# Performance work log

Hardware: AMD Instinct MI355X
Metric: run time of the kernel (lower is better)

Reference implementation:

```python
import jax, jax.numpy as jnp
import numpy as np

N_DIS = 5000
N_GEN = 20000
N = N_DIS + N_GEN
E = 400000
N_MIRNA = 2000
EMB = 128
HID = 64


def setup_inputs() -> dict:
    key = jax.random.key(0)
    ks = jax.random.split(key, 20)
    def g(k, shape, scale=0.05):
        return jax.random.normal(k, shape, dtype=jnp.float32) * scale
    return {
        'd_features': g(ks[0], (N_DIS, 383), 1.0),
        'g_features': g(ks[1], (N_GEN, 4395), 1.0),
        'miRNA_dis': jax.random.uniform(ks[2], (N_MIRNA, N_DIS), dtype=jnp.float32),
        'gene_dis': jax.random.uniform(ks[3], (N_GEN, N_DIS), dtype=jnp.float32),
        'Wd': g(ks[4], (383, EMB)),
        'bd': jnp.zeros((EMB,), jnp.float32),
        'Wg': g(ks[5], (4395, EMB)),
        'bg': jnp.zeros((EMB,), jnp.float32),
        'W1': g(ks[6], (N_MIRNA, EMB)),
        'W4': g(ks[7], (N_DIS, EMB)),
        'Ws1': g(ks[8], (EMB, HID)),
        'Wn1': g(ks[9], (EMB, HID)),
        'b1': jnp.zeros((HID,), jnp.float32),
        'Ws2': g(ks[10], (HID, HID)),
        'Wn2': g(ks[11], (HID, HID)),
        'b2': jnp.zeros((HID,), jnp.float32),
        'src': jax.random.randint(ks[12], (E,), 0, N, dtype=jnp.int32),
        'dst': jax.random.randint(ks[13], (E,), 0, N, dtype=jnp.int32),
    }


def _sage_mean(h, src, dst, Ws, Wn, b):
    # DGL SAGEConv 'mean': fc_self(h) + fc_neigh(mean over in-neighbors) + bias
    msg = h[src]                                            # [E, d] gather
    agg = jax.ops.segment_sum(msg, dst, num_segments=N)     # [N, d] scatter-add
    deg = jax.ops.segment_sum(jnp.ones((dst.shape[0],), h.dtype), dst, num_segments=N)
    neigh = agg / jnp.maximum(deg, 1.0)[:, None]            # mean (zero-deg -> 0)
    return h @ Ws + neigh @ Wn + b


def reference(d_features, g_features, miRNA_dis, gene_dis, Wd, bd, Wg, bg,
              W1, W4, Ws1, Wn1, b1, Ws2, Wn2, b2, src, dst):
    # CrossCompressUnit outputs used by forward: A2 = M1^T W1, B1 = M2 W4
    A2 = miRNA_dis.T @ W1          # [N_DIS, EMB]
    B1 = gene_dis @ W4             # [N_GEN, EMB]
    # Node embeddings (dropout is identity at inference; torch.no_grad block)
    h_dis = 0.9 * (d_features @ Wd + bd) + 0.1 * A2   # [N_DIS, EMB]
    h_gen = 0.9 * (g_features @ Wg + bg) + 0.1 * B1   # [N_GEN, EMB]
    h = jnp.concatenate([h_dis, h_gen], axis=0)        # [N, EMB]
    h = _sage_mean(h, src, dst, Ws1, Wn1, b1)          # [N, 64]
    h = jax.nn.relu(h)
    h = _sage_mean(h, src, dst, Ws2, Wn2, b2)          # [N, 64]
    return h
```

## Files before the change

kernel.cpp:

```cpp
#include <hip/hip_runtime.h>

#define NDIS 5000
#define NGEN 20000
#define NTOT 25000
#define EDG  400000

typedef __attribute__((ext_vector_type(8))) short short8;
typedef __attribute__((ext_vector_type(4))) float f32x4;
typedef __attribute__((ext_vector_type(4), aligned(4))) float f32x4u;
typedef __attribute__((ext_vector_type(4))) unsigned int uint4v;
typedef __attribute__((ext_vector_type(2))) unsigned int uint2v;
typedef __attribute__((ext_vector_type(2), aligned(4))) unsigned int uint2a;

constexpr size_t AL(size_t x) { return (x + 255) & ~(size_t)255; }
constexpr size_t OFF_H0   = 0;
constexpr size_t OFF_PQ   = AL(OFF_H0  + (size_t)NTOT * 128 * 4);
constexpr size_t OFF_H1   = AL(OFF_PQ  + (size_t)NTOT * 128 * 4);
constexpr size_t OFF_DEG  = AL(OFF_H1  + (size_t)NTOT * 128 * 4);
constexpr size_t OFF_RS   = AL(OFF_DEG + (size_t)NTOT * 4);
constexpr size_t OFF_CUR  = AL(OFF_RS  + (size_t)(NTOT + 1) * 4);
constexpr size_t OFF_ESRC = AL(OFF_CUR + (size_t)NTOT * 4);
constexpr size_t OFF_MIT  = AL(OFF_ESRC + (size_t)EDG * 4);
constexpr size_t OFF_BDIS = AL(OFF_MIT + (size_t)5000 * 2048 * 2);
constexpr size_t OFF_BGEN = AL(OFF_BDIS + (size_t)8 * 76 * 512 * 2);
constexpr size_t OFF_BS1  = AL(OFF_BGEN + (size_t)8 * 300 * 512 * 2);
constexpr size_t OFF_BS2  = AL(OFF_BS1 + (size_t)8 * 4 * 512 * 2);

__device__ __forceinline__ ushort f2bf(float f) {
    unsigned u = __float_as_uint(f);
    u += 0x7fffu + ((u >> 16) & 1u);
    return (ushort)(u >> 16);
}

__device__ __forceinline__ unsigned cvtpk(float a, float b) {
    unsigned r;
    asm("v_cvt_pk_bf16_f32 %0, %1, %2" : "=v"(r) : "v"(a), "v"(b));
    return r;
}

__device__ __forceinline__ void MFMA(f32x4& d, short8 a, short8 b) {
    asm volatile("v_mfma_f32_16x16x32_bf16 %0, %1, %2, %0"
                 : "+v"(d) : "v"(a), "v"(b));
}

struct TcvtIns { const float* p[9]; };

__global__ __launch_bounds__(256) void k_tcvt_multi(TcvtIns ins, char* ws)
{
    constexpr int   TR[9]   = {383, 2000, 4395, 5000, 2000, 128, 128, 64, 64};
    constexpr int   TC[9]   = {128, 128, 128, 128, 5000, 64, 64, 64, 64};
    constexpr int   TKT[9]  = {76, 76, 300, 300, 2048 , 4, 4, 4, 4};
    constexpr int   TKO[9]  = {0, 12, 0, 140, 0, 0, 0, 0, 0};
    constexpr int   TRP[9]  = {384, 2048, 4480, 5120, 2048, 128, 128, 128, 128};
    constexpr int   TNOFF[9]= {0, 0, 0, 0, 0, 0, 64, 0, 64};
    constexpr int   TMODE[9]= {1, 1, 1, 1, 0, 1, 1, 1, 1};
    constexpr float TSC[9]  = {0.9f, 0.1f, 0.9f, 0.1f, 1.f, 1.f, 1.f, 1.f, 1.f};
    constexpr size_t TOUT[9]= {OFF_BDIS, OFF_BDIS, OFF_BGEN, OFF_BGEN, OFF_MIT,
                               OFF_BS1, OFF_BS1, OFF_BS2, OFF_BS2};
    constexpr int TNBX[9]   = {4, 4, 4, 4, 157, 2, 2, 2, 2};
    constexpr int PRE[10]   = {0, 48, 304, 864, 1504, 11552, 11560, 11568, 11576, 11584};

    int bid = blockIdx.x;
    int d = 0;
#pragma unroll
    for (int q = 1; q < 9; ++q) if (bid >= PRE[q]) d = q;
    int local = bid - PRE[d];
    int bx = local % TNBX[d], by = local / TNBX[d];
    const int R = TR[d], C = TC[d], KT = TKT[d], KO = TKO[d];
    const int Rp = TRP[d], noff = TNOFF[d];
    const float scale = TSC[d];
    const float* in = ins.p[d];
    ushort* out = (ushort*)(ws + TOUT[d]);

    __shared__ float t[32][33];
    int tx = threadIdx.x & 31, ty = threadIdx.x >> 5;
    int c0 = bx * 32, r0 = by * 32;
#pragma unroll
    for (int j = 0; j < 4; ++j) {
        int r = r0 + ty + j * 8, c = c0 + tx;
        t[ty + j * 8][tx] = (r < R && c < C) ? in[(size_t)r * C + c] : 0.f;
    }
    __syncthreads();
#pragma unroll
    for (int j = 0; j < 4; ++j) {
        int c = c0 + ty + j * 8, r = r0 + tx;
        if (c >= C || r >= Rp) continue;
        ushort bv = f2bf(scale * t[tx][ty + j * 8]);
        if (TMODE[d] == 0) {
            out[(size_t)c * KT + r] = bv;
        } else {
            int n = noff + c, k = r;
            out[(size_t)((n >> 4) * KT + KO + (k >> 5)) * 512 +
                ((k >> 3) & 3) * 128 + (n & 15) * 8 + (k & 7)] = bv;
        }
    }
}

template<int A2MODE, bool ATOMIC>
__global__ __launch_bounds__(256, 2) void gemm_st(
    const float* __restrict__ A1, int lda1, int K1, int nst1,
    const void* __restrict__ A2v, int lda2, int K2, int nst2,
    const ushort* __restrict__ Bf, int KT,
    float* __restrict__ C, int M, const float* __restrict__ bias)
{
    __shared__ ushort lds0[64 * 128];
    __shared__ ushort lds1[64 * 128];
    const int tid  = threadIdx.x;
    const int lane = tid & 63;
    const int w    = tid >> 6;
    const int fr = lane & 15, kq = lane >> 4;
    const int bm0 = blockIdx.x * 64;

    const int NSTT = nst1 + nst2;
    const int per = (NSTT + gridDim.y - 1) / gridDim.y;
    const int s0 = blockIdx.y * per;
    const int s1 = min(NSTT, s0 + per);
    const int NT = s1 - s0;
    if (NT <= 0) return;

    f32x4 acc[4][2];
#pragma unroll
    for (int i = 0; i < 4; ++i) { acc[i][0] = {0.f,0.f,0.f,0.f}; acc[i][1] = {0.f,0.f,0.f,0.f}; }

    uint4v faA[8], faB[8];
    short8 Breg0[4][2], Breg1[4][2];

    const int srow = w * 16 + (lane >> 5);
    const int scol = lane & 31;

    auto issueA = [&](int stg, uint4v* fa) {
        const bool r1 = (A2MODE == 0) || (stg < nst1);
#pragma unroll
        for (int i = 0; i < 8; ++i) {
            int r = bm0 + srow + i * 2;
            if (r > M - 1) r = M - 1;
            if (r1) {
                const int kb = stg << 7;
                const int k = kb + scol * 4;
                const float* p = A1 + (size_t)r * lda1 + k;
                if (kb + 128 <= K1) {
                    fa[i] = __builtin_bit_cast(uint4v, *(const f32x4u*)p);
                } else {
                    f32x4 v;
#pragma unroll
                    for (int e = 0; e < 4; ++e) v[e] = (k + e < K1) ? p[e] : 0.f;
                    fa[i] = __builtin_bit_cast(uint4v, v);
                }
            } else if (A2MODE == 1) {
                const int kb = (stg - nst1) << 7;
                const int kc = kb + scol * 4;
                const float* p = (const float*)A2v + (size_t)r * lda2 + kc;
                if (kb + 128 <= K2) {
                    fa[i] = __builtin_bit_cast(uint4v, *(const f32x4u*)p);
                } else {
                    f32x4 v;
#pragma unroll
                    for (int e = 0; e < 4; ++e) v[e] = (kc + e < K2) ? p[e] : 0.f;
                    fa[i] = __builtin_bit_cast(uint4v, v);
                }
            } else {
                const int kc = ((stg - nst1) << 7) + scol * 4;
                uint2a v = *(const uint2a*)((const ushort*)A2v + (size_t)r * lda2 + kc);
                fa[i][0] = v[0]; fa[i][1] = v[1];
            }
        }
    };
    auto issueB = [&](int stg, short8 (*BR)[2]) {
#pragma unroll
        for (int ks = 0; ks < 4; ++ks)
#pragma unroll
            for (int nf = 0; nf < 2; ++nf)
                BR[ks][nf] = *(const short8*)(
                    Bf + (size_t)((w * 2 + nf) * KT + stg * 4 + ks) * 512 + lane * 8);
    };
    auto writeT = [&](int stg, const uint4v* fa, ushort* buf) {
        const bool cvt = (A2MODE != 2) || (stg < nst1);
        const int G = scol >> 1, h = lane & 1;
#pragma unroll
        for (int i = 0; i < 8; ++i) {
            int r = srow + i * 2;
            const size_t off = (size_t)r * 256 + ((G ^ (r & 7)) << 4) + h * 8;
            uint2v d;
            if (cvt) {
                f32x4 v = __builtin_bit_cast(f32x4, fa[i]);
                d[0] = cvtpk(v[0], v[1]);
                d[1] = cvtpk(v[2], v[3]);
            } else {
                d[0] = fa[i][0]; d[1] = fa[i][1];
            }
            *(uint2v*)((char*)buf + off) = d;
        }
    };

#define PHASE(T, BR, LDSC, FAW, LDSW)                                        \
    {                                                                        \
        const int x7 = fr & 7;                                               \
        _Pragma("unroll")                                                    \
        for (int ks = 0; ks < 4; ++ks) {                                     \
            short8 af[4];                                                    \
            _Pragma("unroll")                                                \
            for (int mf = 0; mf < 4; ++mf)                                   \
                af[mf] = *(const short8*)&LDSC[fr * 128 + mf * 2048 +        \
                                              (((ks * 4 + kq) ^ x7) << 3)];  \
            _Pragma("unroll")                                                \
            for (int mf = 0; mf < 4; ++mf) {                                 \
                MFMA(acc[mf][0], af[mf], BR[ks][0]);                         \
                MFMA(acc[mf][1], af[mf], BR[ks][1]);                         \
            }                                                                \
        }                                                                    \
        if ((T) + 2 < NT) issueB(s0 + (T) + 2, BR);                          \
        __builtin_amdgcn_s_barrier();                                        \
        if ((T) + 1 < NT) {                                                  \
            writeT(s0 + (T) + 1, FAW, LDSW);                                 \
            if ((T) + 3 < NT) issueA(s0 + (T) + 3, FAW);                     \
            asm volatile("s_waitcnt lgkmcnt(0)" ::: "memory");               \
            __builtin_amdgcn_s_barrier();                                    \
        }                                                                    \
    }

    issueA(s0, faA); issueB(s0, Breg0);
    if (NT > 1) { issueA(s0 + 1, faB); issueB(s0 + 1, Breg1); }
    writeT(s0, faA, lds0);
    if (NT > 2) issueA(s0 + 2, faA);
    asm volatile("s_waitcnt lgkmcnt(0)" ::: "memory");
    __builtin_amdgcn_s_barrier();

    for (int t = 0; t < NT; t += 2) {
        PHASE(t, Breg0, lds0, faB, lds1);
        if (t + 1 < NT) PHASE(t + 1, Breg1, lds1, faA, lds0);
    }
#undef PHASE

    asm volatile("s_nop 7\n\ts_nop 7\n\ts_nop 7" ::: "memory");
#pragma unroll
    for (int mf = 0; mf < 4; ++mf)
#pragma unroll
        for (int nf = 0; nf < 2; ++nf)
#pragma unroll
            for (int r = 0; r < 4; ++r) {
                int row = bm0 + mf * 16 + kq * 4 + r;
                if (row < M) {
                    int col = w * 32 + nf * 16 + fr;
                    if (ATOMIC) {
                        atomicAdd(&C[(size_t)row * 128 + col], acc[mf][nf][r]);
                    } else {
                        float v = acc[mf][nf][r];
                        if (col < 64) v += bias[col];
                        C[(size_t)row * 128 + col] = v;
                    }
                }
            }
}

__global__ void k_binit(float* __restrict__ h0, const float* __restrict__ bd,
                        const float* __restrict__ bg) {
    int i = blockIdx.x * 256 + threadIdx.x;
    if (i >= NTOT * 128) return;
    int col = i & 127;
    h0[i] = 0.9f * ((i >> 7) < NDIS ? bd[col] : bg[col]);
}

__global__ void k_deg(const int* __restrict__ dst, int* __restrict__ deg, int E) {
    int e = blockIdx.x * blockDim.x + threadIdx.x;
    if (e < E) atomicAdd(&deg[dst[e]], 1);
}

__global__ __launch_bounds__(1024) void k_scan(const int* __restrict__ deg,
                                               int* __restrict__ row_start,
                                               int* __restrict__ cursor, int n) {
    __shared__ int wsum[16];
    __shared__ int carry_s;
    int t = threadIdx.x;
    int lane = t & 63, wid = t >> 6;
    if (t == 0) { carry_s = 0; row_start[0] = 0; }
    __syncthreads();
    for (int base = 0; base < n; base += 1024) {
        int i = base + t;
        int v = (i < n) ? deg[i] : 0;
        int x = v;
#pragma unroll
        for (int off = 1; off < 64; off <<= 1) {
            int y = __shfl_up(x, off, 64);
            if (lane >= off) x += y;
        }
        if (lane == 63) wsum[wid] = x;
        __syncthreads();
        if (wid == 0) {
            int s = (lane < 16) ? wsum[lane] : 0;
#pragma unroll
            for (int off = 1; off < 16; off <<= 1) {
                int y = __shfl_up(s, off, 64);
                if (lane >= off) s += y;
            }
            if (lane < 16) wsum[lane] = s;
        }
        __syncthreads();
        int pre = (wid > 0 ? wsum[wid - 1] : 0) + carry_s;
        int incl = x + pre;
        if (i < n) { row_start[i + 1] = incl; cursor[i] = incl - v; }
        __syncthreads();
        if (t == 1023) carry_s = incl;
        __syncthreads();
    }
}

__global__ void k_fill(const int* __restrict__ src, const int* __restrict__ dst,
                       int* __restrict__ cursor, int* __restrict__ esrc, int E) {
    int e = blockIdx.x * blockDim.x + threadIdx.x;
    if (e < E) {
        int pos = atomicAdd(&cursor[dst[e]], 1);
        esrc[pos] = src[e];
    }
}

__global__ __launch_bounds__(64) void k_agg(const float* __restrict__ PQ,
                                            const int* __restrict__ rs,
                                            const int* __restrict__ esrc,
                                            float* __restrict__ out, int ldout, int relu)
{
    int n = blockIdx.x, t = threadIdx.x;
    int s0 = rs[n], s1 = rs[n + 1];
    float a0 = 0.f, a1 = 0.f, a2 = 0.f, a3 = 0.f;
    int i = s0;
    for (; i + 4 <= s1; i += 4) {
        int e0 = esrc[i], e1 = esrc[i + 1], e2 = esrc[i + 2], e3 = esrc[i + 3];
        a0 += PQ[(size_t)e0 * 128 + 64 + t];
        a1 += PQ[(size_t)e1 * 128 + 64 + t];
        a2 += PQ[(size_t)e2 * 128 + 64 + t];
        a3 += PQ[(size_t)e3 * 128 + 64 + t];
    }
    for (; i < s1; ++i) a0 += PQ[(size_t)esrc[i] * 128 + 64 + t];
    float s = (a0 + a1) + (a2 + a3);
    float dg = (float)(s1 - s0);
    s /= fmaxf(dg, 1.f);
    float v = PQ[(size_t)n * 128 + t] + s;
    if (relu) v = fmaxf(v, 0.f);
    out[(size_t)n * ldout + t] = v;
}

extern "C" void kernel_launch(void* const* d_in, const int* in_sizes, int n_in,
                              void* d_out, int out_size, void* d_ws, size_t ws_size,
                              hipStream_t stream)
{
    const float* d_features = (const float*)d_in[0];
    const float* g_features = (const float*)d_in[1];
    const float* miRNA_dis  = (const float*)d_in[2];
    const float* gene_dis   = (const float*)d_in[3];
    const float* Wd  = (const float*)d_in[4];
    const float* bd  = (const float*)d_in[5];
    const float* Wg  = (const float*)d_in[6];
    const float* bg  = (const float*)d_in[7];
    const float* W1  = (const float*)d_in[8];
    const float* W4  = (const float*)d_in[9];
    const float* Ws1 = (const float*)d_in[10];
    const float* Wn1 = (const float*)d_in[11];
    const float* b1  = (const float*)d_in[12];
    const float* Ws2 = (const float*)d_in[13];
    const float* Wn2 = (const float*)d_in[14];
    const float* b2  = (const float*)d_in[15];
    const int* src = (const int*)d_in[16];
    const int* dst = (const int*)d_in[17];
    (void)in_sizes; (void)n_in; (void)out_size; (void)ws_size;

    char* ws = (char*)d_ws;
    float*  h0   = (float*)(ws + OFF_H0);
    float*  PQ   = (float*)(ws + OFF_PQ);
    float*  h1   = (float*)(ws + OFF_H1);
    int*    deg  = (int*)(ws + OFF_DEG);
    int*    rs   = (int*)(ws + OFF_RS);
    int*    cur  = (int*)(ws + OFF_CUR);
    int*    esrc = (int*)(ws + OFF_ESRC);
    ushort* miT  = (ushort*)(ws + OFF_MIT);
    ushort* Bdis = (ushort*)(ws + OFF_BDIS);
    ushort* Bgen = (ushort*)(ws + OFF_BGEN);
    ushort* Bs1  = (ushort*)(ws + OFF_BS1);
    ushort* Bs2  = (ushort*)(ws + OFF_BS2);

    hipMemsetAsync(deg, 0, (size_t)NTOT * 4, stream);
    hipMemsetAsync(h1, 0, (size_t)NTOT * 128 * 4, stream);
    k_deg<<<(EDG + 255) / 256, 256, 0, stream>>>(dst, deg, EDG);
    k_scan<<<1, 1024, 0, stream>>>(deg, rs, cur, NTOT);
    k_fill<<<(EDG + 255) / 256, 256, 0, stream>>>(src, dst, cur, esrc, EDG);

    TcvtIns ins;
    ins.p[0] = Wd;  ins.p[1] = W1;  ins.p[2] = Wg;  ins.p[3] = W4;
    ins.p[4] = miRNA_dis; ins.p[5] = Ws1; ins.p[6] = Wn1; ins.p[7] = Ws2; ins.p[8] = Wn2;
    k_tcvt_multi<<<11584, 256, 0, stream>>>(ins, ws);

    k_binit<<<(NTOT * 128 + 255) / 256, 256, 0, stream>>>(h0, bd, bg);
    gemm_st<2, true><<<dim3(79, 5), 256, 0, stream>>>(
        d_features, 383, 383, 3,
        miT, 2048, 2048, 16, Bdis, 76, h0, NDIS, nullptr);
    gemm_st<1, true><<<dim3(313, 4), 256, 0, stream>>>(
        g_features, 4395, 4395, 35,
        gene_dis, 5000, 5000, 40, Bgen, 300,
        h0 + (size_t)NDIS * 128, NGEN, nullptr);

    gemm_st<0, false><<<dim3(391, 1), 256, 0, stream>>>(
        h0, 128, 128, 1, nullptr, 0, 0, 0, Bs1, 4, PQ, NTOT, b1);
    k_agg<<<NTOT, 64, 0, stream>>>(PQ, rs, esrc, h1, 128, 1);

    gemm_st<0, false><<<dim3(391, 1), 256, 0, stream>>>(
        h1, 128, 128, 1, nullptr, 0, 0, 0, Bs2, 4, PQ, NTOT, b2);
    k_agg<<<NTOT, 64, 0, stream>>>(PQ, rs, esrc, (float*)d_out, 64, 0);
}
```

Baseline: 373.8 us.

## Replace split-K atomics with partial buffers and a reduce kernel; fuse degree count

```diff
diff --git a/kernel.cpp b/kernel.cpp
--- a/kernel.cpp
+++ b/kernel.cpp
@@ -25,6 +25,8 @@
 constexpr size_t OFF_BGEN = AL(OFF_BDIS + (size_t)8 * 76 * 512 * 2);
 constexpr size_t OFF_BS1  = AL(OFF_BGEN + (size_t)8 * 300 * 512 * 2);
 constexpr size_t OFF_BS2  = AL(OFF_BS1 + (size_t)8 * 4 * 512 * 2);
+constexpr size_t OFF_PD   = AL(OFF_BS2 + (size_t)8 * 4 * 512 * 2);
+constexpr size_t OFF_PG   = AL(OFF_PD + (size_t)5 * NDIS * 128 * 4);
 
 __device__ __forceinline__ ushort f2bf(float f) {
     unsigned u = __float_as_uint(f);
@@ -45,7 +47,9 @@
 
 struct TcvtIns { const float* p[9]; };
 
-__global__ __launch_bounds__(256) void k_tcvt_multi(TcvtIns ins, char* ws)
+__global__ __launch_bounds__(256) void k_tcvt_multi(TcvtIns ins, char* ws,
+                                                    const int* __restrict__ dst,
+                                                    int* __restrict__ deg)
 {
     constexpr int   TR[9]   = {383, 2000, 4395, 5000, 2000, 128, 128, 64, 64};
     constexpr int   TC[9]   = {128, 128, 128, 128, 5000, 64, 64, 64, 64};
@@ -61,6 +65,11 @@
     constexpr int PRE[10]   = {0, 48, 304, 864, 1504, 11552, 11560, 11568, 11576, 11584};
 
     int bid = blockIdx.x;
+    if (bid >= 11584) {
+        int e = (bid - 11584) * 256 + threadIdx.x;
+        if (e < EDG) atomicAdd(&deg[dst[e]], 1);
+        return;
+    }
     int d = 0;
 #pragma unroll
     for (int q = 1; q < 9; ++q) if (bid >= PRE[q]) d = q;
@@ -96,7 +105,7 @@
     }
 }
 
-template<int A2MODE, bool ATOMIC>
+template<int A2MODE, bool PARTIAL>
 __global__ __launch_bounds__(256, 2) void gemm_st(
     const float* __restrict__ A1, int lda1, int K1, int nst1,
     const void* __restrict__ A2v, int lda2, int K2, int nst2,
@@ -232,6 +241,7 @@
 #undef PHASE
 
     asm volatile("s_nop 7\n\ts_nop 7\n\ts_nop 7" ::: "memory");
+    float* Cs = PARTIAL ? (C + (size_t)blockIdx.y * ((size_t)M * 128)) : C;
 #pragma unroll
     for (int mf = 0; mf < 4; ++mf)
 #pragma unroll
@@ -241,28 +251,37 @@
                 int row = bm0 + mf * 16 + kq * 4 + r;
                 if (row < M) {
                     int col = w * 32 + nf * 16 + fr;
-                    if (ATOMIC) {
-                        atomicAdd(&C[(size_t)row * 128 + col], acc[mf][nf][r]);
+                    if (PARTIAL) {
+                        Cs[(size_t)row * 128 + col] = acc[mf][nf][r];
                     } else {
                         float v = acc[mf][nf][r];
                         if (col < 64) v += bias[col];
-                        C[(size_t)row * 128 + col] = v;
+                        Cs[(size_t)row * 128 + col] = v;
                     }
                 }
             }
 }
 
-__global__ void k_binit(float* __restrict__ h0, const float* __restrict__ bd,
-                        const float* __restrict__ bg) {
+__global__ __launch_bounds__(256) void k_reduce(
+    const float* __restrict__ Pd, const float* __restrict__ Pg,
+    const float* __restrict__ bd, const float* __restrict__ bg,
+    float* __restrict__ h0)
+{
     int i = blockIdx.x * 256 + threadIdx.x;
     if (i >= NTOT * 128) return;
-    int col = i & 127;
-    h0[i] = 0.9f * ((i >> 7) < NDIS ? bd[col] : bg[col]);
-}
-
-__global__ void k_deg(const int* __restrict__ dst, int* __restrict__ deg, int E) {
-    int e = blockIdx.x * blockDim.x + threadIdx.x;
-    if (e < E) atomicAdd(&deg[dst[e]], 1);
+    int row = i >> 7, c = i & 127;
+    float v;
+    if (row < NDIS) {
+        v = 0.9f * bd[c];
+#pragma unroll
+        for (int s = 0; s < 5; ++s) v += Pd[(size_t)s * NDIS * 128 + i];
+    } else {
+        v = 0.9f * bg[c];
+        int j = i - NDIS * 128;
+#pragma unroll
+        for (int s = 0; s < 4; ++s) v += Pg[(size_t)s * NGEN * 128 + j];
+    }
+    h0[i] = v;
 }
 
 __global__ __launch_bounds__(1024) void k_scan(const int* __restrict__ deg,
@@ -375,26 +394,27 @@
     ushort* Bgen = (ushort*)(ws + OFF_BGEN);
     ushort* Bs1  = (ushort*)(ws + OFF_BS1);
     ushort* Bs2  = (ushort*)(ws + OFF_BS2);
+    float*  Pd   = (float*)(ws + OFF_PD);
+    float*  Pg   = (float*)(ws + OFF_PG);
 
     hipMemsetAsync(deg, 0, (size_t)NTOT * 4, stream);
     hipMemsetAsync(h1, 0, (size_t)NTOT * 128 * 4, stream);
-    k_deg<<<(EDG + 255) / 256, 256, 0, stream>>>(dst, deg, EDG);
-    k_scan<<<1, 1024, 0, stream>>>(deg, rs, cur, NTOT);
-    k_fill<<<(EDG + 255) / 256, 256, 0, stream>>>(src, dst, cur, esrc, EDG);
 
     TcvtIns ins;
     ins.p[0] = Wd;  ins.p[1] = W1;  ins.p[2] = Wg;  ins.p[3] = W4;
     ins.p[4] = miRNA_dis; ins.p[5] = Ws1; ins.p[6] = Wn1; ins.p[7] = Ws2; ins.p[8] = Wn2;
-    k_tcvt_multi<<<11584, 256, 0, stream>>>(ins, ws);
-
-    k_binit<<<(NTOT * 128 + 255) / 256, 256, 0, stream>>>(h0, bd, bg);
+    k_tcvt_multi<<<11584 + 1563, 256, 0, stream>>>(ins, ws, dst, deg);
+
+    k_scan<<<1, 1024, 0, stream>>>(deg, rs, cur, NTOT);
+    k_fill<<<(EDG + 255) / 256, 256, 0, stream>>>(src, dst, cur, esrc, EDG);
+
     gemm_st<2, true><<<dim3(79, 5), 256, 0, stream>>>(
         d_features, 383, 383, 3,
-        miT, 2048, 2048, 16, Bdis, 76, h0, NDIS, nullptr);
+        miT, 2048, 2048, 16, Bdis, 76, Pd, NDIS, nullptr);
     gemm_st<1, true><<<dim3(313, 4), 256, 0, stream>>>(
         g_features, 4395, 4395, 35,
-        gene_dis, 5000, 5000, 40, Bgen, 300,
-        h0 + (size_t)NDIS * 128, NGEN, nullptr);
+        gene_dis, 5000, 5000, 40, Bgen, 300, Pg, NGEN, nullptr);
+    k_reduce<<<(NTOT * 128 + 255) / 256, 256, 0, stream>>>(Pd, Pg, bd, bg, h0);
 
     gemm_st<0, false><<<dim3(391, 1), 256, 0, stream>>>(
         h0, 128, 128, 1, nullptr, 0, 0, 0, Bs1, 4, PQ, NTOT, b1);
```

Measured after the change: 379.5 us. No clear change (+1.5%).

## Fuse degree count into transpose kernel and parallelize prefix scan

Applied to the files above, without the earlier changes.

```diff
diff --git a/kernel.cpp b/kernel.cpp
--- a/kernel.cpp
+++ b/kernel.cpp
@@ -19,7 +19,10 @@
 constexpr size_t OFF_DEG  = AL(OFF_H1  + (size_t)NTOT * 128 * 4);
 constexpr size_t OFF_RS   = AL(OFF_DEG + (size_t)NTOT * 4);
 constexpr size_t OFF_CUR  = AL(OFF_RS  + (size_t)(NTOT + 1) * 4);
-constexpr size_t OFF_ESRC = AL(OFF_CUR + (size_t)NTOT * 4);
+constexpr size_t OFF_TMP  = AL(OFF_CUR + (size_t)NTOT * 4);
+constexpr size_t OFF_BSUM = AL(OFF_TMP + (size_t)NTOT * 4);
+constexpr size_t OFF_BOFF = AL(OFF_BSUM + 64 * 4);
+constexpr size_t OFF_ESRC = AL(OFF_BOFF + 64 * 4);
 constexpr size_t OFF_MIT  = AL(OFF_ESRC + (size_t)EDG * 4);
 constexpr size_t OFF_BDIS = AL(OFF_MIT + (size_t)5000 * 2048 * 2);
 constexpr size_t OFF_BGEN = AL(OFF_BDIS + (size_t)8 * 76 * 512 * 2);
@@ -45,7 +48,9 @@
 
 struct TcvtIns { const float* p[9]; };
 
-__global__ __launch_bounds__(256) void k_tcvt_multi(TcvtIns ins, char* ws)
+__global__ __launch_bounds__(256) void k_tcvt_multi(TcvtIns ins, char* ws,
+                                                    const int* __restrict__ dst,
+                                                    int* __restrict__ deg)
 {
     constexpr int   TR[9]   = {383, 2000, 4395, 5000, 2000, 128, 128, 64, 64};
     constexpr int   TC[9]   = {128, 128, 128, 128, 5000, 64, 64, 64, 64};
@@ -61,6 +66,11 @@
     constexpr int PRE[10]   = {0, 48, 304, 864, 1504, 11552, 11560, 11568, 11576, 11584};
 
     int bid = blockIdx.x;
+    if (bid >= 11584) {
+        int e = (bid - 11584) * 256 + threadIdx.x;
+        if (e < EDG) atomicAdd(&deg[dst[e]], 1);
+        return;
+    }
     int d = 0;
 #pragma unroll
     for (int q = 1; q < 9; ++q) if (bid >= PRE[q]) d = q;
@@ -260,47 +270,59 @@
     h0[i] = 0.9f * ((i >> 7) < NDIS ? bd[col] : bg[col]);
 }
 
-__global__ void k_deg(const int* __restrict__ dst, int* __restrict__ deg, int E) {
-    int e = blockIdx.x * blockDim.x + threadIdx.x;
-    if (e < E) atomicAdd(&deg[dst[e]], 1);
-}
-
-__global__ __launch_bounds__(1024) void k_scan(const int* __restrict__ deg,
-                                               int* __restrict__ row_start,
-                                               int* __restrict__ cursor, int n) {
+__global__ __launch_bounds__(1024) void k_scan1(const int* __restrict__ deg,
+                                                int* __restrict__ tmp,
+                                                int* __restrict__ bsum, int n) {
     __shared__ int wsum[16];
-    __shared__ int carry_s;
+    int t = threadIdx.x, lane = t & 63, wid = t >> 6;
+    int i = blockIdx.x * 1024 + t;
+    int v = (i < n) ? deg[i] : 0;
+    int x = v;
+#pragma unroll
+    for (int off = 1; off < 64; off <<= 1) {
+        int y = __shfl_up(x, off, 64);
+        if (lane >= off) x += y;
+    }
+    if (lane == 63) wsum[wid] = x;
+    __syncthreads();
+    if (wid == 0) {
+        int s = (lane < 16) ? wsum[lane] : 0;
+#pragma unroll
+        for (int off = 1; off < 16; off <<= 1) {
+            int y = __shfl_up(s, off, 64);
+            if (lane >= off) s += y;
+        }
+        if (lane < 16) wsum[lane] = s;
+    }
+    __syncthreads();
+    int incl = x + (wid > 0 ? wsum[wid - 1] : 0);
+    if (i < n) tmp[i] = incl;
+    if (t == 1023) bsum[blockIdx.x] = incl;
+}
+
+__global__ void k_scan2(const int* __restrict__ bsum, int* __restrict__ boff, int nb) {
     int t = threadIdx.x;
-    int lane = t & 63, wid = t >> 6;
-    if (t == 0) { carry_s = 0; row_start[0] = 0; }
-    __syncthreads();
-    for (int base = 0; base < n; base += 1024) {
-        int i = base + t;
-        int v = (i < n) ? deg[i] : 0;
-        int x = v;
-#pragma unroll
-        for (int off = 1; off < 64; off <<= 1) {
-            int y = __shfl_up(x, off, 64);
-            if (lane >= off) x += y;
-        }
-        if (lane == 63) wsum[wid] = x;
-        __syncthreads();
-        if (wid == 0) {
-            int s = (lane < 16) ? wsum[lane] : 0;
-#pragma unroll
-            for (int off = 1; off < 16; off <<= 1) {
-                int y = __shfl_up(s, off, 64);
-                if (lane >= off) s += y;
-            }
-            if (lane < 16) wsum[lane] = s;
-        }
-        __syncthreads();
-        int pre = (wid > 0 ? wsum[wid - 1] : 0) + carry_s;
-        int incl = x + pre;
-        if (i < n) { row_start[i + 1] = incl; cursor[i] = incl - v; }
-        __syncthreads();
-        if (t == 1023) carry_s = incl;
-        __syncthreads();
+    int v = (t < nb) ? bsum[t] : 0;
+    int x = v;
+#pragma unroll
+    for (int off = 1; off < 64; off <<= 1) {
+        int y = __shfl_up(x, off, 64);
+        if (t >= off) x += y;
+    }
+    if (t < nb) boff[t] = x - v;
+}
+
+__global__ __launch_bounds__(1024) void k_scan3(const int* __restrict__ deg,
+                                                const int* __restrict__ tmp,
+                                                const int* __restrict__ boff,
+                                                int* __restrict__ rs,
+                                                int* __restrict__ cursor, int n) {
+    int i = blockIdx.x * 1024 + threadIdx.x;
+    if (i == 0) rs[0] = 0;
+    if (i < n) {
+        int v = tmp[i] + boff[blockIdx.x];
+        rs[i + 1] = v;
+        cursor[i] = v - deg[i];
     }
 }
 
@@ -369,6 +391,9 @@
     int*    deg  = (int*)(ws + OFF_DEG);
     int*    rs   = (int*)(ws + OFF_RS);
     int*    cur  = (int*)(ws + OFF_CUR);
+    int*    tmp  = (int*)(ws + OFF_TMP);
+    int*    bsum = (int*)(ws + OFF_BSUM);
+    int*    boff = (int*)(ws + OFF_BOFF);
     int*    esrc = (int*)(ws + OFF_ESRC);
     ushort* miT  = (ushort*)(ws + OFF_MIT);
     ushort* Bdis = (ushort*)(ws + OFF_BDIS);
@@ -378,14 +403,16 @@
 
     hipMemsetAsync(deg, 0, (size_t)NTOT * 4, stream);
     hipMemsetAsync(h1, 0, (size_t)NTOT * 128 * 4, stream);
-    k_deg<<<(EDG + 255) / 256, 256, 0, stream>>>(dst, deg, EDG);
-    k_scan<<<1, 1024, 0, stream>>>(deg, rs, cur, NTOT);
-    k_fill<<<(EDG + 255) / 256, 256, 0, stream>>>(src, dst, cur, esrc, EDG);
 
     TcvtIns ins;
     ins.p[0] = Wd;  ins.p[1] = W1;  ins.p[2] = Wg;  ins.p[3] = W4;
     ins.p[4] = miRNA_dis; ins.p[5] = Ws1; ins.p[6] = Wn1; ins.p[7] = Ws2; ins.p[8] = Wn2;
-    k_tcvt_multi<<<11584, 256, 0, stream>>>(ins, ws);
+    k_tcvt_multi<<<11584 + 1563, 256, 0, stream>>>(ins, ws, dst, deg);
+
+    k_scan1<<<25, 1024, 0, stream>>>(deg, tmp, bsum, NTOT);
+    k_scan2<<<1, 64, 0, stream>>>(bsum, boff, 25);
+    k_scan3<<<25, 1024, 0, stream>>>(deg, tmp, boff, rs, cur, NTOT);
+    k_fill<<<(EDG + 255) / 256, 256, 0, stream>>>(src, dst, cur, esrc, EDG);
 
     k_binit<<<(NTOT * 128 + 255) / 256, 256, 0, stream>>>(h0, bd, bg);
     gemm_st<2, true><<<dim3(79, 5), 256, 0, stream>>>(
```

New measurement: 351.6 us. 5.9% less time.
